# Kernel optimization log

Measured on AMD Instinct MI355X. Metric: run time of the kernel, lower is better.

The kernel has to match this reference:

```python
import jax, jax.numpy as jnp
import numpy as np

DIM = 256
EPS = 1e-8


def rmsnorm(y, scale):
    # full RMSNorm (p < 0): rms = ||y||_2 / sqrt(d)
    norm = jnp.linalg.norm(y, axis=-1, keepdims=True)
    rms = norm * (DIM ** -0.5)
    return scale * (y / (rms + EPS))


def setup_inputs() -> dict:
    key = jax.random.key(0)
    ks = jax.random.split(key, 12)
    d = DIM
    inp = {
        "agent": jax.random.normal(ks[0], (64, d), dtype=jnp.float32),
        "x": jax.random.normal(ks[1], (8, 8192, d), dtype=jnp.float32),
        "W_qkv": jax.random.normal(ks[2], (3 * d, d), dtype=jnp.float32) * 0.02,
        "b_qkv": jnp.zeros((3 * d,), dtype=jnp.float32),
        "W_agent": jax.random.normal(ks[3], (2 * d, d), dtype=jnp.float32) * 0.02,
        "b_agent": jnp.zeros((2 * d,), dtype=jnp.float32),
        "W_fc1": jax.random.normal(ks[4], (d, d), dtype=jnp.float32) * 0.02,
        "b_fc1": jnp.zeros((d,), dtype=jnp.float32),
        "W_fc2": jax.random.normal(ks[5], (d, d), dtype=jnp.float32) * 0.02,
        "b_fc2": jnp.zeros((d,), dtype=jnp.float32),
        "norm_scale": jnp.ones((d,), dtype=jnp.float32),
    }
    return inp


def reference(agent, x, W_qkv, b_qkv, W_agent, b_agent, W_fc1, b_fc1, W_fc2, b_fc2, norm_scale):
    sc = DIM ** -0.5
    # qkv projection of x: [B, N, 3d] -> q, k, v each [B, N, d]
    qkv = x @ W_qkv.T + b_qkv
    q, k, v = jnp.split(qkv, 3, axis=-1)
    # agent projection: [K, 2d] -> q_agent, k_agent each [K, d]
    qa_ka = agent @ W_agent.T + b_agent
    q_agent, k_agent = jnp.split(qa_ka, 2, axis=-1)
    # stage 1: agents attend over tokens  -> [B, K, N]
    attn1 = jax.nn.softmax(jnp.einsum('kd,bnd->bkn', q_agent, k) * sc, axis=-1)
    v1 = jnp.einsum('bkn,bnd->bkd', attn1, v)  # [B, K, d]
    v1 = v1 @ W_fc1.T + b_fc1
    # stage 2: tokens attend over agents -> [B, N, K]
    attn2 = jax.nn.softmax(jnp.einsum('bnd,kd->bnk', q, k_agent) * sc, axis=-1)
    v2 = jnp.einsum('bnk,bkd->bnd', attn2, v1)  # [B, N, d]
    v2 = v2 @ W_fc2.T + b_fc2
    return rmsnorm(v2 + x, norm_scale)
```

## Files before the change

kernel.cpp:

```cpp
#include <hip/hip_runtime.h>
#include <hip/hip_bf16.h>

typedef __attribute__((ext_vector_type(4))) float f32x4;
typedef __attribute__((ext_vector_type(8))) short s16x8;
typedef __attribute__((ext_vector_type(4))) short s16x4;

__device__ __forceinline__ unsigned short f2bf(float f) {
    unsigned int u; __builtin_memcpy(&u, &f, 4);
    u += 0x7fffu + ((u >> 16) & 1u);
    return (unsigned short)(u >> 16);
}
__device__ __forceinline__ float bf2f(unsigned short h) {
    unsigned int u = ((unsigned int)h) << 16;
    float f; __builtin_memcpy(&f, &u, 4);
    return f;
}
__device__ __forceinline__ s16x8 pack8(f32x4 a, f32x4 b) {
    s16x8 r;
    r[0] = (short)f2bf(a[0]); r[1] = (short)f2bf(a[1]);
    r[2] = (short)f2bf(a[2]); r[3] = (short)f2bf(a[3]);
    r[4] = (short)f2bf(b[0]); r[5] = (short)f2bf(b[1]);
    r[6] = (short)f2bf(b[2]); r[7] = (short)f2bf(b[3]);
    return r;
}

template<bool AF32, bool BF32, bool OUTBF16, bool BIAS>
__global__ __launch_bounds__(256) void gemm_k256(
    const void* __restrict__ Ap, long sA, long bAstr,
    const void* __restrict__ Bp, long sB,
    const float* __restrict__ bias,
    void* __restrict__ Cp, long sC, long bCstr,
    int M, int N)
{
    __shared__ alignas(16) unsigned short As[128 * 256];
    __shared__ alignas(16) unsigned short Bs[64 * 256];
    const int tid = threadIdx.x;
    const int lane = tid & 63;
    const int w = tid >> 6;
    const int m0 = blockIdx.x * 128;
    const int nt = blockIdx.y;
    const int z = blockIdx.z;

    {
        const int kk = (tid & 31) * 8;
        #pragma unroll
        for (int j = 0; j < 16; ++j) {
            const int row = (tid >> 5) + j * 8;
            int rowg = m0 + row; if (rowg > M - 1) rowg = M - 1;
            s16x8 v;
            if constexpr (AF32) {
                const float* s = (const float*)Ap + (size_t)z * bAstr + (size_t)rowg * sA + kk;
                f32x4 f0 = *(const f32x4*)s;
                f32x4 f1 = *(const f32x4*)(s + 4);
                v = pack8(f0, f1);
            } else {
                const unsigned short* s = (const unsigned short*)Ap + (size_t)z * bAstr + (size_t)rowg * sA + kk;
                v = *(const s16x8*)s;
            }
            *(s16x8*)((char*)As + row * 512 + ((kk * 2) ^ ((row & 7) << 4))) = v;
        }
        #pragma unroll
        for (int j = 0; j < 8; ++j) {
            const int row = (tid >> 5) + j * 8;
            const int rowg = nt * 64 + row;
            s16x8 v;
            if constexpr (BF32) {
                const float* s = (const float*)Bp + (size_t)rowg * sB + kk;
                f32x4 f0 = *(const f32x4*)s;
                f32x4 f1 = *(const f32x4*)(s + 4);
                v = pack8(f0, f1);
            } else {
                const unsigned short* s = (const unsigned short*)Bp + (size_t)rowg * sB + kk;
                v = *(const s16x8*)s;
            }
            *(s16x8*)((char*)Bs + row * 512 + ((kk * 2) ^ ((row & 7) << 4))) = v;
        }
    }
    __syncthreads();

    f32x4 acc[2][4];
    const f32x4 zero = {0.f, 0.f, 0.f, 0.f};
    #pragma unroll
    for (int rf = 0; rf < 2; ++rf)
        #pragma unroll
        for (int cf = 0; cf < 4; ++cf)
            acc[rf][cf] = zero;

    #pragma unroll
    for (int ks = 0; ks < 8; ++ks) {
        const int kb = ks * 64 + ((lane >> 4) << 4);
        s16x8 areg[2], bfr[4];
        #pragma unroll
        for (int rf = 0; rf < 2; ++rf) {
            const int row = w * 32 + rf * 16 + (lane & 15);
            areg[rf] = *(const s16x8*)((const char*)As + row * 512 + (kb ^ ((row & 7) << 4)));
        }
        #pragma unroll
        for (int cf = 0; cf < 4; ++cf) {
            const int row = cf * 16 + (lane & 15);
            bfr[cf] = *(const s16x8*)((const char*)Bs + row * 512 + (kb ^ ((row & 7) << 4)));
        }
        #pragma unroll
        for (int rf = 0; rf < 2; ++rf)
            #pragma unroll
            for (int cf = 0; cf < 4; ++cf)
                acc[rf][cf] = __builtin_amdgcn_mfma_f32_16x16x32_bf16(
                    areg[rf], bfr[cf], acc[rf][cf], 0, 0, 0);
    }

    #pragma unroll
    for (int cf = 0; cf < 4; ++cf) {
        const int n = nt * 64 + cf * 16 + (lane & 15);
        const float bv = BIAS ? bias[n] : 0.f;
        #pragma unroll
        for (int rf = 0; rf < 2; ++rf) {
            #pragma unroll
            for (int r = 0; r < 4; ++r) {
                const int m = m0 + w * 32 + rf * 16 + ((lane >> 4) << 2) + r;
                if (m < M) {
                    const float v = acc[rf][cf][r] + bv;
                    const size_t co = (size_t)z * bCstr + (size_t)m * sC + n;
                    if constexpr (OUTBF16) ((unsigned short*)Cp)[co] = f2bf(v);
                    else                   ((float*)Cp)[co] = v;
                }
            }
        }
    }
}

__global__ __launch_bounds__(256) void build_M2(
    const float* __restrict__ W_qkv, const float* __restrict__ b_qkv,
    const float* __restrict__ agent, const float* __restrict__ W_agent,
    const float* __restrict__ b_agent,
    unsigned short* __restrict__ MS, float* __restrict__ cbias)
{
    const int i = blockIdx.x;
    const int t = threadIdx.x;
    __shared__ float ag[256];
    __shared__ float qs[256];
    const int a = i & 63;
    const bool isS1 = (i < 64);
    ag[t] = agent[(size_t)a * 256 + t];
    __syncthreads();
    const int tp = isS1 ? t : 256 + t;
    {
        const float* wr = W_agent + (size_t)tp * 256;
        float q = 0.f;
        #pragma unroll 4
        for (int d = 0; d < 256; d += 4) {
            f32x4 wv = *(const f32x4*)(wr + d);
            q += ag[d] * wv[0] + ag[d + 1] * wv[1] + ag[d + 2] * wv[2] + ag[d + 3] * wv[3];
        }
        qs[t] = (q + b_agent[tp]) * 0.0625f;
    }
    __syncthreads();
    const float* W  = W_qkv + (isS1 ? 256 * 256 : 0);
    const float* bb = b_qkv + (isS1 ? 256 : 0);
    float acc = 0.f, cb = 0.f;
    for (int dout = 0; dout < 256; ++dout) {
        const float q = qs[dout];
        acc += q * W[(size_t)dout * 256 + t];
        cb  += q * bb[dout];
    }
    MS[i * 256 + t] = f2bf(acc);
    if (t == 0) cbias[i] = cb;
}

__global__ __launch_bounds__(256) void xproj2(
    const float* __restrict__ x,
    const unsigned short* __restrict__ MS,
    const float* __restrict__ cbias,
    float* __restrict__ S1T,
    float* __restrict__ S2,
    float* __restrict__ mpart, float* __restrict__ lpart)
{
    __shared__ alignas(16) unsigned short As[64 * 256];
    const int tid = threadIdx.x, lane = tid & 63, w = tid >> 6;
    const int lr = lane & 15, lq = lane >> 4;
    const long m0 = (long)blockIdx.x * 64;

    {
        const int k0 = (tid & 31) * 8;
        #pragma unroll
        for (int j = 0; j < 8; ++j) {
            const int row = (tid >> 5) + j * 8;
            const float* s = x + (m0 + row) * 256 + k0;
            f32x4 f0 = *(const f32x4*)s;
            f32x4 f1 = *(const f32x4*)(s + 4);
            *(s16x8*)((char*)As + row * 512 + ((k0 * 2) ^ ((row & 7) << 4))) = pack8(f0, f1);
        }
    }
    __syncthreads();

    f32x4 acc[4][2];
    const f32x4 zero = {0.f, 0.f, 0.f, 0.f};
    #pragma unroll
    for (int rf = 0; rf < 4; ++rf)
        #pragma unroll
        for (int j = 0; j < 2; ++j)
            acc[rf][j] = zero;

    #pragma unroll
    for (int ks = 0; ks < 8; ++ks) {
        const int kb = ks * 64 + lq * 16;
        s16x8 areg[4];
        #pragma unroll
        for (int rf = 0; rf < 4; ++rf) {
            const int row = rf * 16 + lr;
            areg[rf] = *(const s16x8*)((const char*)As + row * 512 + (kb ^ ((row & 7) << 4)));
        }
        s16x8 bfr[2];
        #pragma unroll
        for (int j = 0; j < 2; ++j) {
            const int msrow = j * 64 + w * 16 + lr;
            bfr[j] = *(const s16x8*)((const char*)MS + (size_t)msrow * 512 + kb);
        }
        #pragma unroll
        for (int rf = 0; rf < 4; ++rf)
            #pragma unroll
            for (int j = 0; j < 2; ++j)
                acc[rf][j] = __builtin_amdgcn_mfma_f32_16x16x32_bf16(
                    areg[rf], bfr[j], acc[rf][j], 0, 0, 0);
    }

    #pragma unroll
    for (int j = 0; j < 2; ++j) {
        const int a = w * 16 + lr;
        const float bv = cbias[j * 64 + a];
        float* dst = j ? S2 : S1T;
        float mx = -1e30f;
        #pragma unroll
        for (int rf = 0; rf < 4; ++rf)
            #pragma unroll
            for (int r = 0; r < 4; ++r) {
                const float v = acc[rf][j][r] + bv;
                dst[(m0 + rf * 16 + lq * 4 + r) * 64 + a] = v;
                mx = fmaxf(mx, v);
            }
        if (j == 0) {
            mx = fmaxf(mx, __shfl_xor(mx, 16));
            mx = fmaxf(mx, __shfl_xor(mx, 32));
            float sm = 0.f;
            #pragma unroll
            for (int rf = 0; rf < 4; ++rf)
                #pragma unroll
                for (int r = 0; r < 4; ++r)
                    sm += __expf(acc[rf][j][r] + bv - mx);
            sm += __shfl_xor(sm, 16);
            sm += __shfl_xor(sm, 32);
            if (lq == 0) {
                mpart[(size_t)blockIdx.x * 64 + a] = mx;
                lpart[(size_t)blockIdx.x * 64 + a] = sm;
            }
        }
    }
}

__global__ __launch_bounds__(256) void pv_mfma2(
    const float* __restrict__ S1T,
    const float* __restrict__ x,
    const float* __restrict__ mpart,
    const float* __restrict__ lpart,
    float* __restrict__ y_part)
{
    __shared__ alignas(16) unsigned short P_lds[64 * 128];
    __shared__ alignas(16) unsigned short XT[128 * 136];
    const int tid = threadIdx.x, lane = tid & 63, w = tid >> 6;
    const int lr = lane & 15, lq = lane >> 4;
    const int c = blockIdx.x, dh = blockIdx.y, b = blockIdx.z;
    const int a4 = (tid & 15) * 4;

    f32x4 m4, l4;
    {
        float* scratch = (float*)XT;
        const int a = tid & 63, s4 = tid >> 6;
        const size_t bb = (size_t)b * 128;
        float M = -1e30f;
        for (int cc = s4; cc < 128; cc += 4)
            M = fmaxf(M, mpart[(bb + cc) * 64 + a]);
        float L = 0.f;
        for (int cc = s4; cc < 128; cc += 4) {
            const size_t idx = (bb + cc) * 64 + a;
            L += lpart[idx] * __expf(mpart[idx] - M);
        }
        scratch[tid] = M;
        scratch[256 + tid] = L;
        __syncthreads();
        if (tid < 64) {
            float Mm = scratch[tid];
            #pragma unroll
            for (int ss = 1; ss < 4; ++ss) Mm = fmaxf(Mm, scratch[ss * 64 + tid]);
            float Ll = 0.f;
            #pragma unroll
            for (int ss = 0; ss < 4; ++ss)
                Ll += scratch[256 + ss * 64 + tid] * __expf(scratch[ss * 64 + tid] - Mm);
            scratch[512 + tid] = Mm;
            scratch[576 + tid] = 1.0f / Ll;
        }
        __syncthreads();
        #pragma unroll
        for (int j = 0; j < 4; ++j) {
            m4[j] = scratch[512 + a4 + j];
            l4[j] = scratch[576 + a4 + j];
        }
        __syncthreads();
    }

    f32x4 acc[4][2];
    const f32x4 zero = {0.f, 0.f, 0.f, 0.f};
    #pragma unroll
    for (int rf = 0; rf < 4; ++rf)
        #pragma unroll
        for (int cf = 0; cf < 2; ++cf)
            acc[rf][cf] = zero;

    for (int kt = 0; kt < 2; ++kt) {
        const size_t ng0 = (size_t)b * 8192 + c * 256 + kt * 128;
        #pragma unroll
        for (int pass = 0; pass < 4; ++pass) {
            const int np = 2 * (tid >> 4) + pass * 32;
            const float* s = S1T + (ng0 + np) * 64 + a4;
            f32x4 s0 = *(const f32x4*)s;
            f32x4 s1 = *(const f32x4*)(s + 64);
            #pragma unroll
            for (int j = 0; j < 4; ++j) {
                const int a = a4 + j;
                const float p0 = __expf(s0[j] - m4[j]) * l4[j];
                const float p1 = __expf(s1[j] - m4[j]) * l4[j];
                const unsigned int pk = (unsigned int)f2bf(p0) | ((unsigned int)f2bf(p1) << 16);
                *(unsigned int*)((char*)P_lds + a * 256 + ((np * 2) ^ (((a >> 1) & 7) << 4))) = pk;
            }
        }
        {
            const int nh = tid >> 2;
            const int dq = tid & 3;
            const float* xbase = x + (ng0 + 2 * nh) * 256 + dh * 128;
            #pragma unroll
            for (int pass = 0; pass < 8; ++pass) {
                const int dl0 = pass * 16 + dq * 4;
                f32x4 xa = *(const f32x4*)(xbase + dl0);
                f32x4 xb = *(const f32x4*)(xbase + 256 + dl0);
                #pragma unroll
                for (int jj = 0; jj < 4; ++jj) {
                    const unsigned int pk = (unsigned int)f2bf(xa[jj]) | ((unsigned int)f2bf(xb[jj]) << 16);
                    *(unsigned int*)((char*)XT + (dl0 + jj) * 272 + nh * 4) = pk;
                }
            }
        }
        __syncthreads();
        #pragma unroll
        for (int ks = 0; ks < 4; ++ks) {
            const int kbn = ks * 64 + lq * 16;
            s16x8 af[4], bfv[2];
            #pragma unroll
            for (int rf = 0; rf < 4; ++rf) {
                const int row = rf * 16 + lr;
                af[rf] = *(const s16x8*)((const char*)P_lds + row * 256 + (kbn ^ (((row >> 1) & 7) << 4)));
            }
            #pragma unroll
            for (int cf = 0; cf < 2; ++cf) {
                const int dl = w * 32 + cf * 16 + lr;
                bfv[cf] = *(const s16x8*)((const char*)XT + dl * 272 + kbn);
            }
            #pragma unroll
            for (int rf = 0; rf < 4; ++rf)
                #pragma unroll
                for (int cf = 0; cf < 2; ++cf)
                    acc[rf][cf] = __builtin_amdgcn_mfma_f32_16x16x32_bf16(
                        af[rf], bfv[cf], acc[rf][cf], 0, 0, 0);
        }
        __syncthreads();
    }
    #pragma unroll
    for (int rf = 0; rf < 4; ++rf)
        #pragma unroll
        for (int cf = 0; cf < 2; ++cf)
            #pragma unroll
            for (int r = 0; r < 4; ++r) {
                const int a = rf * 16 + lq * 4 + r;
                const int d = dh * 128 + w * 32 + cf * 16 + lr;
                y_part[(((size_t)b * 32 + c) * 64 + a) * 256 + d] = acc[rf][cf][r];
            }
}

__global__ void v1_reduce(const float* __restrict__ y_part,
                          unsigned short* __restrict__ y_rawb)
{
    const int a = blockIdx.x, b = blockIdx.y, t = threadIdx.x;
    f32x4 s = {0.f, 0.f, 0.f, 0.f};
    for (int c = 0; c < 32; ++c)
        s += *(const f32x4*)&y_part[(((size_t)b * 32 + c) * 64 + a) * 256 + t * 4];
    s16x4 pk;
    #pragma unroll
    for (int j = 0; j < 4; ++j) pk[j] = (short)f2bf(s[j]);
    *(s16x4*)&y_rawb[((size_t)b * 64 + a) * 256 + t * 4] = pk;
}

__global__ __launch_bounds__(256) void stage2_final(const float* __restrict__ S2,
                                                    const float* __restrict__ uu,
                                                    const float* __restrict__ x,
                                                    const float* __restrict__ nscale,
                                                    float* __restrict__ out)
{
    __shared__ alignas(16) unsigned short uT[256 * 64];
    __shared__ alignas(16) unsigned short P[64 * 64];
    __shared__ float ssq[4][64];
    const int tid = threadIdx.x, lane = tid & 63, w = tid >> 6;
    const int lr = lane & 15, lq = lane >> 4;
    const int b = blockIdx.x >> 7;
    const long n0 = (long)blockIdx.x * 64;

    {
        const int pr = tid >> 3;
        const int sub = tid & 7;
        const float* u0 = uu + ((size_t)b * 64 + 2 * pr) * 256;
        #pragma unroll
        for (int pass = 0; pass < 8; ++pass) {
            const int d0 = pass * 32 + sub * 4;
            f32x4 ua = *(const f32x4*)(u0 + d0);
            f32x4 ub = *(const f32x4*)(u0 + 256 + d0);
            #pragma unroll
            for (int jj = 0; jj < 4; ++jj) {
                const int d = d0 + jj;
                const unsigned int pk = (unsigned int)f2bf(ua[jj]) | ((unsigned int)f2bf(ub[jj]) << 16);
                *(unsigned int*)((char*)uT + d * 128 + ((pr * 4) ^ ((d & 7) << 4))) = pk;
            }
        }
    }
    {
        const int t = lane >> 2, q = lane & 3;
        const int nl = w * 16 + t;
        const float* srow = S2 + (n0 + nl) * 64 + q * 16;
        f32x4 sv[4];
        #pragma unroll
        for (int j = 0; j < 4; ++j) sv[j] = *(const f32x4*)(srow + j * 4);
        float mx = -1e30f;
        #pragma unroll
        for (int j = 0; j < 4; ++j)
            #pragma unroll
            for (int e = 0; e < 4; ++e) mx = fmaxf(mx, sv[j][e]);
        mx = fmaxf(mx, __shfl_xor(mx, 1));
        mx = fmaxf(mx, __shfl_xor(mx, 2));
        float p[16];
        float sm = 0.f;
        #pragma unroll
        for (int j = 0; j < 4; ++j)
            #pragma unroll
            for (int e = 0; e < 4; ++e) {
                p[j * 4 + e] = __expf(sv[j][e] - mx);
                sm += p[j * 4 + e];
            }
        sm += __shfl_xor(sm, 1);
        sm += __shfl_xor(sm, 2);
        const float rs = 1.f / sm;
        s16x8 o0, o1;
        #pragma unroll
        for (int e = 0; e < 8; ++e) o0[e] = (short)f2bf(p[e] * rs);
        #pragma unroll
        for (int e = 0; e < 8; ++e) o1[e] = (short)f2bf(p[8 + e] * rs);
        const int swz = (nl & 7) << 4;
        *(s16x8*)((char*)P + nl * 128 + ((q * 32) ^ swz)) = o0;
        *(s16x8*)((char*)P + nl * 128 + ((q * 32 + 16) ^ swz)) = o1;
    }
    __syncthreads();

    f32x4 acc[4][4];
    const f32x4 zero = {0.f, 0.f, 0.f, 0.f};
    #pragma unroll
    for (int rf = 0; rf < 4; ++rf)
        #pragma unroll
        for (int cf = 0; cf < 4; ++cf)
            acc[rf][cf] = zero;
    #pragma unroll
    for (int ks = 0; ks < 2; ++ks) {
        const int kb = ks * 64 + lq * 16;
        s16x8 af[4], bfv[4];
        #pragma unroll
        for (int rf = 0; rf < 4; ++rf) {
            const int dR = w * 64 + rf * 16 + lr;
            af[rf] = *(const s16x8*)((const char*)uT + dR * 128 + (kb ^ ((dR & 7) << 4)));
        }
        #pragma unroll
        for (int cf = 0; cf < 4; ++cf) {
            const int nR = cf * 16 + lr;
            bfv[cf] = *(const s16x8*)((const char*)P + nR * 128 + (kb ^ ((nR & 7) << 4)));
        }
        #pragma unroll
        for (int rf = 0; rf < 4; ++rf)
            #pragma unroll
            for (int cf = 0; cf < 4; ++cf)
                acc[rf][cf] = __builtin_amdgcn_mfma_f32_16x16x32_bf16(
                    af[rf], bfv[cf], acc[rf][cf], 0, 0, 0);
    }

    float part[4] = {0.f, 0.f, 0.f, 0.f};
    #pragma unroll
    for (int cf = 0; cf < 4; ++cf) {
        const long n = n0 + cf * 16 + lr;
        #pragma unroll
        for (int rf = 0; rf < 4; ++rf) {
            const int d0 = w * 64 + rf * 16 + lq * 4;
            const f32x4 xr = *(const f32x4*)&x[n * 256 + d0];
            acc[rf][cf] += xr;
            part[cf] += acc[rf][cf][0] * acc[rf][cf][0] + acc[rf][cf][1] * acc[rf][cf][1]
                      + acc[rf][cf][2] * acc[rf][cf][2] + acc[rf][cf][3] * acc[rf][cf][3];
        }
    }
    #pragma unroll
    for (int cf = 0; cf < 4; ++cf) {
        float s = part[cf];
        s += __shfl_xor(s, 16);
        s += __shfl_xor(s, 32);
        if (lq == 0) ssq[w][cf * 16 + lr] = s;
    }
    __syncthreads();

    #pragma unroll
    for (int cf = 0; cf < 4; ++cf) {
        const int tokl = cf * 16 + lr;
        const float tot = ssq[0][tokl] + ssq[1][tokl] + ssq[2][tokl] + ssq[3][tokl];
        const float inv = 1.f / (sqrtf(tot) * 0.0625f + 1e-8f);
        const long n = n0 + tokl;
        #pragma unroll
        for (int rf = 0; rf < 4; ++rf) {
            const int d0 = w * 64 + rf * 16 + lq * 4;
            const f32x4 sc4 = *(const f32x4*)&nscale[d0];
            f32x4 o = sc4 * acc[rf][cf] * inv;
            *(f32x4*)&out[n * 256 + d0] = o;
        }
    }
}

extern "C" void kernel_launch(void* const* d_in, const int* in_sizes, int n_in,
                              void* d_out, int out_size, void* d_ws, size_t ws_size,
                              hipStream_t stream)
{
    const float* agent   = (const float*)d_in[0];
    const float* x       = (const float*)d_in[1];
    const float* W_qkv   = (const float*)d_in[2];
    const float* b_qkv   = (const float*)d_in[3];
    const float* W_agent = (const float*)d_in[4];
    const float* b_agent = (const float*)d_in[5];
    const float* W_fc1   = (const float*)d_in[6];
    const float* b_fc1   = (const float*)d_in[7];
    const float* W_fc2   = (const float*)d_in[8];
    const float* b_fc2   = (const float*)d_in[9];
    const float* nscale  = (const float*)d_in[10];
    float* out = (float*)d_out;

    char* wsp = (char*)d_ws;
    size_t off = 0;
    auto alloc = [&](size_t n) { void* p = wsp + off; off += (n + 255) & ~(size_t)255; return p; };

    unsigned short* MS = (unsigned short*)alloc(128UL * 256 * 2);
    float*  cbias  = (float*)alloc(128UL * 4);
    float*  S1T    = (float*)alloc(65536UL * 64 * 4);
    float*  S2     = (float*)alloc(65536UL * 64 * 4);
    float*  mpart  = (float*)alloc(1024UL * 64 * 4);
    float*  lpart  = (float*)alloc(1024UL * 64 * 4);
    float*  y_part = (float*)alloc(8UL * 32 * 64 * 256 * 4);
    unsigned short* y_rawb = (unsigned short*)alloc(512UL * 256 * 2);
    unsigned short* t0b    = (unsigned short*)alloc(512UL * 256 * 2);
    unsigned short* t1b    = (unsigned short*)alloc(512UL * 256 * 2);
    float*  uu     = (float*)alloc(512UL * 256 * 4);

    build_M2<<<128, 256, 0, stream>>>(W_qkv, b_qkv, agent, W_agent, b_agent, MS, cbias);
    xproj2<<<1024, 256, 0, stream>>>(x, MS, cbias, S1T, S2, mpart, lpart);
    pv_mfma2<<<dim3(32, 2, 8), 256, 0, stream>>>(S1T, x, mpart, lpart, y_part);
    v1_reduce<<<dim3(64, 8), 64, 0, stream>>>(y_part, y_rawb);
    gemm_k256<false, true, true, true><<<dim3(4, 4, 1), 256, 0, stream>>>(
        y_rawb, 256, 0, W_qkv + 512 * 256, 256, b_qkv + 512, t0b, 256, 0, 512, 256);
    gemm_k256<false, true, true, true><<<dim3(4, 4, 1), 256, 0, stream>>>(
        t0b, 256, 0, W_fc1, 256, b_fc1, t1b, 256, 0, 512, 256);
    gemm_k256<false, true, false, true><<<dim3(4, 4, 1), 256, 0, stream>>>(
        t1b, 256, 0, W_fc2, 256, b_fc2, uu, 256, 0, 512, 256);
    stage2_final<<<1024, 256, 0, stream>>>(S2, uu, x, nscale, out);
}
```

Before: 135.6 us.

## Fuse reduce and three small GEMMs into one kernel; precompute stage-2 softmax probs

Replaces the v1_reduce kernel and three separate small GEMM launches with a single chain_fused kernel, one block per batch, that reduces the partial sums and runs the three bf16 GEMMs back to back in shared memory. The weights for those GEMMs are converted to bf16 ahead of time by extra blocks in build_M2. The stage-2 softmax moves into xproj2, which now writes bf16 probabilities instead of fp32 scores, so less intermediate data goes through memory. pv_mfma2 uses half as many chunks, each with more k-steps, which shrinks y_part. The aim is fewer launches and less traffic, but the fused chain runs on only 8 blocks and pv_mfma2 has fewer blocks, so parallelism is lower.

```diff
diff --git a/kernel.cpp b/kernel.cpp
--- a/kernel.cpp
+++ b/kernel.cpp
@@ -24,118 +24,28 @@
     return r;
 }
 
-template<bool AF32, bool BF32, bool OUTBF16, bool BIAS>
-__global__ __launch_bounds__(256) void gemm_k256(
-    const void* __restrict__ Ap, long sA, long bAstr,
-    const void* __restrict__ Bp, long sB,
-    const float* __restrict__ bias,
-    void* __restrict__ Cp, long sC, long bCstr,
-    int M, int N)
-{
-    __shared__ alignas(16) unsigned short As[128 * 256];
-    __shared__ alignas(16) unsigned short Bs[64 * 256];
-    const int tid = threadIdx.x;
-    const int lane = tid & 63;
-    const int w = tid >> 6;
-    const int m0 = blockIdx.x * 128;
-    const int nt = blockIdx.y;
-    const int z = blockIdx.z;
-
-    {
-        const int kk = (tid & 31) * 8;
-        #pragma unroll
-        for (int j = 0; j < 16; ++j) {
-            const int row = (tid >> 5) + j * 8;
-            int rowg = m0 + row; if (rowg > M - 1) rowg = M - 1;
-            s16x8 v;
-            if constexpr (AF32) {
-                const float* s = (const float*)Ap + (size_t)z * bAstr + (size_t)rowg * sA + kk;
-                f32x4 f0 = *(const f32x4*)s;
-                f32x4 f1 = *(const f32x4*)(s + 4);
-                v = pack8(f0, f1);
-            } else {
-                const unsigned short* s = (const unsigned short*)Ap + (size_t)z * bAstr + (size_t)rowg * sA + kk;
-                v = *(const s16x8*)s;
-            }
-            *(s16x8*)((char*)As + row * 512 + ((kk * 2) ^ ((row & 7) << 4))) = v;
-        }
-        #pragma unroll
-        for (int j = 0; j < 8; ++j) {
-            const int row = (tid >> 5) + j * 8;
-            const int rowg = nt * 64 + row;
-            s16x8 v;
-            if constexpr (BF32) {
-                const float* s = (const float*)Bp + (size_t)rowg * sB + kk;
-                f32x4 f0 = *(const f32x4*)s;
-                f32x4 f1 = *(const f32x4*)(s + 4);
-                v = pack8(f0, f1);
-            } else {
-                const unsigned short* s = (const unsigned short*)Bp + (size_t)rowg * sB + kk;
-                v = *(const s16x8*)s;
-            }
-            *(s16x8*)((char*)Bs + row * 512 + ((kk * 2) ^ ((row & 7) << 4))) = v;
-        }
-    }
-    __syncthreads();
-
-    f32x4 acc[2][4];
-    const f32x4 zero = {0.f, 0.f, 0.f, 0.f};
-    #pragma unroll
-    for (int rf = 0; rf < 2; ++rf)
-        #pragma unroll
-        for (int cf = 0; cf < 4; ++cf)
-            acc[rf][cf] = zero;
-
-    #pragma unroll
-    for (int ks = 0; ks < 8; ++ks) {
-        const int kb = ks * 64 + ((lane >> 4) << 4);
-        s16x8 areg[2], bfr[4];
-        #pragma unroll
-        for (int rf = 0; rf < 2; ++rf) {
-            const int row = w * 32 + rf * 16 + (lane & 15);
-            areg[rf] = *(const s16x8*)((const char*)As + row * 512 + (kb ^ ((row & 7) << 4)));
-        }
-        #pragma unroll
-        for (int cf = 0; cf < 4; ++cf) {
-            const int row = cf * 16 + (lane & 15);
-            bfr[cf] = *(const s16x8*)((const char*)Bs + row * 512 + (kb ^ ((row & 7) << 4)));
-        }
-        #pragma unroll
-        for (int rf = 0; rf < 2; ++rf)
-            #pragma unroll
-            for (int cf = 0; cf < 4; ++cf)
-                acc[rf][cf] = __builtin_amdgcn_mfma_f32_16x16x32_bf16(
-                    areg[rf], bfr[cf], acc[rf][cf], 0, 0, 0);
-    }
-
-    #pragma unroll
-    for (int cf = 0; cf < 4; ++cf) {
-        const int n = nt * 64 + cf * 16 + (lane & 15);
-        const float bv = BIAS ? bias[n] : 0.f;
-        #pragma unroll
-        for (int rf = 0; rf < 2; ++rf) {
-            #pragma unroll
-            for (int r = 0; r < 4; ++r) {
-                const int m = m0 + w * 32 + rf * 16 + ((lane >> 4) << 2) + r;
-                if (m < M) {
-                    const float v = acc[rf][cf][r] + bv;
-                    const size_t co = (size_t)z * bCstr + (size_t)m * sC + n;
-                    if constexpr (OUTBF16) ((unsigned short*)Cp)[co] = f2bf(v);
-                    else                   ((float*)Cp)[co] = v;
-                }
-            }
-        }
-    }
-}
-
 __global__ __launch_bounds__(256) void build_M2(
     const float* __restrict__ W_qkv, const float* __restrict__ b_qkv,
     const float* __restrict__ agent, const float* __restrict__ W_agent,
     const float* __restrict__ b_agent,
-    unsigned short* __restrict__ MS, float* __restrict__ cbias)
+    const float* __restrict__ W_fc1, const float* __restrict__ W_fc2,
+    unsigned short* __restrict__ MS, float* __restrict__ cbias,
+    unsigned short* __restrict__ Wb)
 {
     const int i = blockIdx.x;
     const int t = threadIdx.x;
+    if (i >= 128) {
+        const int R0 = (i - 128) * 4;
+        #pragma unroll
+        for (int rr = 0; rr < 4; ++rr) {
+            const int R = R0 + rr;
+            const float* src = (R < 256) ? W_qkv + (size_t)(512 + R) * 256
+                             : (R < 512) ? W_fc1 + (size_t)(R - 256) * 256
+                                         : W_fc2 + (size_t)(R - 512) * 256;
+            Wb[(size_t)R * 256 + t] = f2bf(src[t]);
+        }
+        return;
+    }
     __shared__ float ag[256];
     __shared__ float qs[256];
     const int a = i & 63;
@@ -171,7 +81,7 @@
     const unsigned short* __restrict__ MS,
     const float* __restrict__ cbias,
     float* __restrict__ S1T,
-    float* __restrict__ S2,
+    unsigned short* __restrict__ P2,
     float* __restrict__ mpart, float* __restrict__ lpart)
 {
     __shared__ alignas(16) unsigned short As[64 * 256];
@@ -223,36 +133,83 @@
                     areg[rf], bfr[j], acc[rf][j], 0, 0, 0);
     }
 
-    #pragma unroll
-    for (int j = 0; j < 2; ++j) {
+    {
         const int a = w * 16 + lr;
-        const float bv = cbias[j * 64 + a];
-        float* dst = j ? S2 : S1T;
+        const float bv = cbias[a];
         float mx = -1e30f;
         #pragma unroll
         for (int rf = 0; rf < 4; ++rf)
             #pragma unroll
             for (int r = 0; r < 4; ++r) {
-                const float v = acc[rf][j][r] + bv;
-                dst[(m0 + rf * 16 + lq * 4 + r) * 64 + a] = v;
+                const float v = acc[rf][0][r] + bv;
+                S1T[(m0 + rf * 16 + lq * 4 + r) * 64 + a] = v;
                 mx = fmaxf(mx, v);
             }
-        if (j == 0) {
-            mx = fmaxf(mx, __shfl_xor(mx, 16));
-            mx = fmaxf(mx, __shfl_xor(mx, 32));
-            float sm = 0.f;
-            #pragma unroll
-            for (int rf = 0; rf < 4; ++rf)
-                #pragma unroll
-                for (int r = 0; r < 4; ++r)
-                    sm += __expf(acc[rf][j][r] + bv - mx);
-            sm += __shfl_xor(sm, 16);
-            sm += __shfl_xor(sm, 32);
-            if (lq == 0) {
-                mpart[(size_t)blockIdx.x * 64 + a] = mx;
-                lpart[(size_t)blockIdx.x * 64 + a] = sm;
-            }
-        }
+        mx = fmaxf(mx, __shfl_xor(mx, 16));
+        mx = fmaxf(mx, __shfl_xor(mx, 32));
+        float sm = 0.f;
+        #pragma unroll
+        for (int rf = 0; rf < 4; ++rf)
+            #pragma unroll
+            for (int r = 0; r < 4; ++r)
+                sm += __expf(acc[rf][0][r] + bv - mx);
+        sm += __shfl_xor(sm, 16);
+        sm += __shfl_xor(sm, 32);
+        if (lq == 0) {
+            mpart[(size_t)blockIdx.x * 64 + a] = mx;
+            lpart[(size_t)blockIdx.x * 64 + a] = sm;
+        }
+    }
+
+    __syncthreads();
+    {
+        float* SC = (float*)As;
+        const int a = w * 16 + lr;
+        const float bv = cbias[64 + a];
+        #pragma unroll
+        for (int rf = 0; rf < 4; ++rf)
+            #pragma unroll
+            for (int r = 0; r < 4; ++r) {
+                const int n = rf * 16 + lq * 4 + r;
+                SC[n * 68 + a] = acc[rf][1][r] + bv;
+            }
+    }
+    __syncthreads();
+    {
+        const float* SC = (const float*)As;
+        const int t4 = lane >> 2, q = lane & 3;
+        const int nl = w * 16 + t4;
+        f32x4 sv[4];
+        #pragma unroll
+        for (int j = 0; j < 4; ++j) sv[j] = *(const f32x4*)&SC[nl * 68 + q * 16 + j * 4];
+        float mx = -1e30f;
+        #pragma unroll
+        for (int j = 0; j < 4; ++j)
+            #pragma unroll
+            for (int e = 0; e < 4; ++e) mx = fmaxf(mx, sv[j][e]);
+        mx = fmaxf(mx, __shfl_xor(mx, 1));
+        mx = fmaxf(mx, __shfl_xor(mx, 2));
+        float p[16];
+        float sm = 0.f;
+        #pragma unroll
+        for (int j = 0; j < 4; ++j)
+            #pragma unroll
+            for (int e = 0; e < 4; ++e) {
+                p[j * 4 + e] = __expf(sv[j][e] - mx);
+                sm += p[j * 4 + e];
+            }
+        sm += __shfl_xor(sm, 1);
+        sm += __shfl_xor(sm, 2);
+        const float rs = 1.f / sm;
+        s16x8 o0, o1;
+        #pragma unroll
+        for (int e = 0; e < 8; ++e) o0[e] = (short)f2bf(p[e] * rs);
+        #pragma unroll
+        for (int e = 0; e < 8; ++e) o1[e] = (short)f2bf(p[8 + e] * rs);
+        const int swz = (nl & 7) << 4;
+        char* row = (char*)P2 + (m0 + nl) * 128;
+        *(s16x8*)(row + ((q * 32) ^ swz)) = o0;
+        *(s16x8*)(row + ((q * 32 + 16) ^ swz)) = o1;
     }
 }
 
@@ -314,8 +271,8 @@
         for (int cf = 0; cf < 2; ++cf)
             acc[rf][cf] = zero;
 
-    for (int kt = 0; kt < 2; ++kt) {
-        const size_t ng0 = (size_t)b * 8192 + c * 256 + kt * 128;
+    for (int kt = 0; kt < 4; ++kt) {
+        const size_t ng0 = (size_t)b * 8192 + c * 512 + kt * 128;
         #pragma unroll
         for (int pass = 0; pass < 4; ++pass) {
             const int np = 2 * (tid >> 4) + pass * 32;
@@ -379,24 +336,115 @@
             for (int r = 0; r < 4; ++r) {
                 const int a = rf * 16 + lq * 4 + r;
                 const int d = dh * 128 + w * 32 + cf * 16 + lr;
-                y_part[(((size_t)b * 32 + c) * 64 + a) * 256 + d] = acc[rf][cf][r];
-            }
-}
-
-__global__ void v1_reduce(const float* __restrict__ y_part,
-                          unsigned short* __restrict__ y_rawb)
+                y_part[(((size_t)b * 16 + c) * 64 + a) * 256 + d] = acc[rf][cf][r];
+            }
+}
+
+__global__ __launch_bounds__(256) void chain_fused(
+    const float* __restrict__ y_part,
+    const unsigned short* __restrict__ Wb,
+    const float* __restrict__ b_qkv,
+    const float* __restrict__ b_fc1,
+    const float* __restrict__ b_fc2,
+    float* __restrict__ uu)
 {
-    const int a = blockIdx.x, b = blockIdx.y, t = threadIdx.x;
-    f32x4 s = {0.f, 0.f, 0.f, 0.f};
-    for (int c = 0; c < 32; ++c)
-        s += *(const f32x4*)&y_part[(((size_t)b * 32 + c) * 64 + a) * 256 + t * 4];
-    s16x4 pk;
-    #pragma unroll
-    for (int j = 0; j < 4; ++j) pk[j] = (short)f2bf(s[j]);
-    *(s16x4*)&y_rawb[((size_t)b * 64 + a) * 256 + t * 4] = pk;
-}
-
-__global__ __launch_bounds__(256) void stage2_final(const float* __restrict__ S2,
+    __shared__ alignas(16) unsigned short A0[64 * 256];
+    __shared__ alignas(16) unsigned short A1[64 * 256];
+    const int tid = threadIdx.x, lane = tid & 63, w = tid >> 6;
+    const int lr = lane & 15, lq = lane >> 4;
+    const int b = blockIdx.x;
+
+    {
+        const float* yp = y_part + (size_t)b * 16 * 64 * 256;
+        f32x4 r16[16];
+        const f32x4 zero = {0.f, 0.f, 0.f, 0.f};
+        #pragma unroll
+        for (int j = 0; j < 16; ++j) r16[j] = zero;
+        for (int c = 0; c < 16; ++c) {
+            const float* base = yp + (size_t)c * 16384 + tid * 4;
+            #pragma unroll
+            for (int j = 0; j < 16; ++j)
+                r16[j] += *(const f32x4*)(base + j * 1024);
+        }
+        #pragma unroll
+        for (int j = 0; j < 16; ++j) {
+            const int a = j * 4 + (tid >> 6);
+            const int d0 = (tid & 63) * 4;
+            s16x4 pk;
+            #pragma unroll
+            for (int e = 0; e < 4; ++e) pk[e] = (short)f2bf(r16[j][e]);
+            *(s16x4*)((char*)A0 + a * 512 + ((d0 * 2) ^ ((a & 7) << 4))) = pk;
+        }
+    }
+    __syncthreads();
+
+    unsigned short* bufA = A0;
+    unsigned short* bufB = A1;
+    for (int s = 0; s < 3; ++s) {
+        const unsigned short* W = Wb + (size_t)s * 65536;
+        const float* bias = (s == 0) ? (b_qkv + 512) : (s == 1) ? b_fc1 : b_fc2;
+        f32x4 acc[4][4];
+        const f32x4 zero = {0.f, 0.f, 0.f, 0.f};
+        #pragma unroll
+        for (int rf = 0; rf < 4; ++rf)
+            #pragma unroll
+            for (int cf = 0; cf < 4; ++cf)
+                acc[rf][cf] = zero;
+        #pragma unroll
+        for (int ks = 0; ks < 8; ++ks) {
+            const int kb = ks * 64 + lq * 16;
+            s16x8 af[4], bf[4];
+            #pragma unroll
+            for (int rf = 0; rf < 4; ++rf) {
+                const int row = rf * 16 + lr;
+                af[rf] = *(const s16x8*)((const char*)bufA + row * 512 + (kb ^ ((row & 7) << 4)));
+            }
+            #pragma unroll
+            for (int cf = 0; cf < 4; ++cf) {
+                const int col = w * 64 + cf * 16 + lr;
+                bf[cf] = *(const s16x8*)((const char*)W + (size_t)col * 512 + kb);
+            }
+            #pragma unroll
+            for (int rf = 0; rf < 4; ++rf)
+                #pragma unroll
+                for (int cf = 0; cf < 4; ++cf)
+                    acc[rf][cf] = __builtin_amdgcn_mfma_f32_16x16x32_bf16(
+                        af[rf], bf[cf], acc[rf][cf], 0, 0, 0);
+        }
+        if (s < 2) {
+            #pragma unroll
+            for (int cf = 0; cf < 4; ++cf) {
+                const int col = w * 64 + cf * 16 + lr;
+                const float bv = bias[col];
+                #pragma unroll
+                for (int rf = 0; rf < 4; ++rf)
+                    #pragma unroll
+                    for (int r = 0; r < 4; ++r) {
+                        const int a = rf * 16 + lq * 4 + r;
+                        *(unsigned short*)((char*)bufB + a * 512 + ((col * 2) ^ ((a & 7) << 4)))
+                            = f2bf(acc[rf][cf][r] + bv);
+                    }
+            }
+            __syncthreads();
+            unsigned short* t = bufA; bufA = bufB; bufB = t;
+        } else {
+            #pragma unroll
+            for (int cf = 0; cf < 4; ++cf) {
+                const int col = w * 64 + cf * 16 + lr;
+                const float bv = bias[col];
+                #pragma unroll
+                for (int rf = 0; rf < 4; ++rf)
+                    #pragma unroll
+                    for (int r = 0; r < 4; ++r) {
+                        const int a = rf * 16 + lq * 4 + r;
+                        uu[((size_t)b * 64 + a) * 256 + col] = acc[rf][cf][r] + bv;
+                    }
+            }
+        }
+    }
+}
+
+__global__ __launch_bounds__(256) void stage2_final(const unsigned short* __restrict__ P2,
                                                     const float* __restrict__ uu,
                                                     const float* __restrict__ x,
                                                     const float* __restrict__ nscale,
@@ -428,39 +476,12 @@
         }
     }
     {
-        const int t = lane >> 2, q = lane & 3;
-        const int nl = w * 16 + t;
-        const float* srow = S2 + (n0 + nl) * 64 + q * 16;
-        f32x4 sv[4];
-        #pragma unroll
-        for (int j = 0; j < 4; ++j) sv[j] = *(const f32x4*)(srow + j * 4);
-        float mx = -1e30f;
-        #pragma unroll
-        for (int j = 0; j < 4; ++j)
-            #pragma unroll
-            for (int e = 0; e < 4; ++e) mx = fmaxf(mx, sv[j][e]);
-        mx = fmaxf(mx, __shfl_xor(mx, 1));
-        mx = fmaxf(mx, __shfl_xor(mx, 2));
-        float p[16];
-        float sm = 0.f;
-        #pragma unroll
-        for (int j = 0; j < 4; ++j)
-            #pragma unroll
-            for (int e = 0; e < 4; ++e) {
-                p[j * 4 + e] = __expf(sv[j][e] - mx);
-                sm += p[j * 4 + e];
-            }
-        sm += __shfl_xor(sm, 1);
-        sm += __shfl_xor(sm, 2);
-        const float rs = 1.f / sm;
-        s16x8 o0, o1;
-        #pragma unroll
-        for (int e = 0; e < 8; ++e) o0[e] = (short)f2bf(p[e] * rs);
-        #pragma unroll
-        for (int e = 0; e < 8; ++e) o1[e] = (short)f2bf(p[8 + e] * rs);
-        const int swz = (nl & 7) << 4;
-        *(s16x8*)((char*)P + nl * 128 + ((q * 32) ^ swz)) = o0;
-        *(s16x8*)((char*)P + nl * 128 + ((q * 32 + 16) ^ swz)) = o1;
+        const int row = tid & 63, seg = tid >> 6;
+        const char* src = (const char*)P2 + (n0 + row) * 128 + seg * 32;
+        s16x8 v0 = *(const s16x8*)src;
+        s16x8 v1 = *(const s16x8*)(src + 16);
+        *(s16x8*)((char*)P + row * 128 + seg * 32) = v0;
+        *(s16x8*)((char*)P + row * 128 + seg * 32 + 16) = v1;
     }
     __syncthreads();
 
@@ -554,25 +575,18 @@
 
     unsigned short* MS = (unsigned short*)alloc(128UL * 256 * 2);
     float*  cbias  = (float*)alloc(128UL * 4);
+    unsigned short* Wb = (unsigned short*)alloc(3UL * 256 * 256 * 2);
     float*  S1T    = (float*)alloc(65536UL * 64 * 4);
-    float*  S2     = (float*)alloc(65536UL * 64 * 4);
+    unsigned short* P2 = (unsigned short*)alloc(65536UL * 64 * 2);
     float*  mpart  = (float*)alloc(1024UL * 64 * 4);
     float*  lpart  = (float*)alloc(1024UL * 64 * 4);
-    float*  y_part = (float*)alloc(8UL * 32 * 64 * 256 * 4);
-    unsigned short* y_rawb = (unsigned short*)alloc(512UL * 256 * 2);
-    unsigned short* t0b    = (unsigned short*)alloc(512UL * 256 * 2);
-    unsigned short* t1b    = (unsigned short*)alloc(512UL * 256 * 2);
+    float*  y_part = (float*)alloc(8UL * 16 * 64 * 256 * 4);
     float*  uu     = (float*)alloc(512UL * 256 * 4);
 
-    build_M2<<<128, 256, 0, stream>>>(W_qkv, b_qkv, agent, W_agent, b_agent, MS, cbias);
-    xproj2<<<1024, 256, 0, stream>>>(x, MS, cbias, S1T, S2, mpart, lpart);
-    pv_mfma2<<<dim3(32, 2, 8), 256, 0, stream>>>(S1T, x, mpart, lpart, y_part);
-    v1_reduce<<<dim3(64, 8), 64, 0, stream>>>(y_part, y_rawb);
-    gemm_k256<false, true, true, true><<<dim3(4, 4, 1), 256, 0, stream>>>(
-        y_rawb, 256, 0, W_qkv + 512 * 256, 256, b_qkv + 512, t0b, 256, 0, 512, 256);
-    gemm_k256<false, true, true, true><<<dim3(4, 4, 1), 256, 0, stream>>>(
-        t0b, 256, 0, W_fc1, 256, b_fc1, t1b, 256, 0, 512, 256);
-    gemm_k256<false, true, false, true><<<dim3(4, 4, 1), 256, 0, stream>>>(
-        t1b, 256, 0, W_fc2, 256, b_fc2, uu, 256, 0, 512, 256);
-    stage2_final<<<1024, 256, 0, stream>>>(S2, uu, x, nscale, out);
-}
+    build_M2<<<320, 256, 0, stream>>>(W_qkv, b_qkv, agent, W_agent, b_agent,
+                                      W_fc1, W_fc2, MS, cbias, Wb);
+    xproj2<<<1024, 256, 0, stream>>>(x, MS, cbias, S1T, P2, mpart, lpart);
+    pv_mfma2<<<dim3(16, 2, 8), 256, 0, stream>>>(S1T, x, mpart, lpart, y_part);
+    chain_fused<<<8, 256, 0, stream>>>(y_part, Wb, b_qkv, b_fc1, b_fc2, uu);
+    stage2_final<<<1024, 256, 0, stream>>>(P2, uu, x, nscale, out);
+}
```

After: 138.9 us. 2.5% more time.
